# Optimization experiments

Hardware: AMD Instinct MI355X
Metric: run time of the kernel (lower is better)

Reference implementation:

```python
import jax, jax.numpy as jnp
import numpy as np

NUM_NODES = 1_000_000
H_DIM = 64
OUT_DIM = 32
NUM_RELS = 64
NUM_BASES = 4
N_SRC0 = 400_000
N_DST1 = 100_000
N_DST2 = 20_000
E1 = 600_000
E2 = 300_000


def setup_inputs() -> dict:
    key = jax.random.key(0)
    ks = jax.random.split(key, 16)
    inp = {
        "input_nodes": jax.random.randint(ks[0], (N_SRC0,), 0, NUM_NODES),
        "src1": jax.random.randint(ks[1], (E1,), 0, N_SRC0),
        "dst1": jax.random.randint(ks[2], (E1,), 0, N_DST1),
        "etype1": jax.random.randint(ks[3], (E1,), 0, NUM_RELS),
        "norm1": jax.random.uniform(ks[4], (E1, 1), dtype=jnp.float32),
        "src2": jax.random.randint(ks[5], (E2,), 0, N_DST1),
        "dst2": jax.random.randint(ks[6], (E2,), 0, N_DST2),
        "etype2": jax.random.randint(ks[7], (E2,), 0, NUM_RELS),
        "norm2": jax.random.uniform(ks[8], (E2, 1), dtype=jnp.float32),
        # learned parameters
        "emb": jax.random.normal(ks[9], (NUM_NODES, H_DIM), dtype=jnp.float32),
        "V1": jax.random.normal(ks[10], (NUM_BASES, H_DIM, H_DIM), dtype=jnp.float32) * 0.05,
        "comp1": jax.random.normal(ks[11], (NUM_RELS, NUM_BASES), dtype=jnp.float32) * 0.3,
        "b1": jnp.zeros((H_DIM,), dtype=jnp.float32),
        "V2": jax.random.normal(ks[12], (NUM_BASES, H_DIM, OUT_DIM), dtype=jnp.float32) * 0.05,
        "comp2": jax.random.normal(ks[13], (NUM_RELS, NUM_BASES), dtype=jnp.float32) * 0.3,
        "b2": jnp.zeros((OUT_DIM,), dtype=jnp.float32),
    }
    return inp


def rel_graph_conv(x, src, dst, etype, norm, V, comp, bias, n_dst):
    """Basis-decomposed RelGraphConv (no self-loop): m_e = (x[src_e] @ W_{etype_e}) * norm_e,
    with W_r = sum_b comp[r,b] V[b]; aggregate by sum into dst nodes, then add bias."""
    xe = x[src]                                 # [E, d] gather of source features
    coeff = comp[etype]                         # [E, B] relation coefficients per edge
    y = jnp.einsum('ed,bdo->ebo', xe, V)        # [E, B, o] feature x each basis
    m = jnp.einsum('ebo,eb->eo', y, coeff)      # [E, o] relation-specific message
    m = m * norm                                # per-edge normalization ([E,1] broadcast)
    h = jax.ops.segment_sum(m, dst, num_segments=n_dst)  # scatter-add to dst
    return h + bias


def reference(input_nodes, src1, dst1, etype1, norm1, src2, dst2, etype2, norm2,
              emb, V1, comp1, b1, V2, comp2, b2):
    x = emb[input_nodes]                                           # [N_src0, h]
    h = rel_graph_conv(x, src1, dst1, etype1, norm1, V1, comp1, b1, N_DST1)
    h = jax.nn.relu(h)
    out = rel_graph_conv(h, src2, dst2, etype2, norm2, V2, comp2, b2, N_DST2)
    return out
```

## Files before the change

kernel.cpp:

```cpp
#include <hip/hip_runtime.h>
#include <stdint.h>

#define NUM_NODES 1000000
#define H_DIM 64
#define OUT_DIM 32
#define NUM_RELS 64
#define NUM_BASES 4
#define N_SRC0 400000
#define N_DST1 100000
#define N_DST2 20000
#define E1 600000
#define E2 300000
#define NDST_TOT (N_DST1 + N_DST2)
#define E_TOT (E1 + E2)

typedef __attribute__((ext_vector_type(8))) short bf16x8;
typedef __attribute__((ext_vector_type(4))) float floatx4;

__device__ __forceinline__ unsigned short f2bf(float f){
  union{float f; unsigned u;} v; v.f=f;
  unsigned u=v.u;
  unsigned r=(u + 0x7FFFu + ((u>>16)&1u))>>16;
  return (unsigned short)r;
}
__device__ __forceinline__ float bf2f(unsigned short h){
  union{unsigned u; float f;} v; v.u=((unsigned)h)<<16; return v.f;
}

__global__ void k_init(const float* __restrict__ V1, const float* __restrict__ V2,
                       ushort* __restrict__ Btab1, ushort* __restrict__ Btab2,
                       int* __restrict__ deg){
  int t = blockIdx.x*blockDim.x + threadIdx.x;
  if (t < NDST_TOT) deg[t] = 0;
  if (t < 16384){
    int j = t & 7, lane = (t>>3)&63, kk = (t>>9)&7, nt = t>>12;
    int kdim = kk*32 + (lane>>4)*8 + j;
    int o = nt*16 + (lane&15);
    int k = kdim>>2, b = kdim&3;
    Btab1[t] = f2bf(V1[(b*64 + k)*64 + o]);
  } else if (t < 24576){
    int u = t - 16384;
    int j = u & 7, lane = (u>>3)&63, kk = (u>>9)&7, nt = u>>12;
    int kdim = kk*32 + (lane>>4)*8 + j;
    int o = nt*16 + (lane&15);
    int k = kdim>>2, b = kdim&3;
    Btab2[u] = f2bf(V2[(b*64 + k)*32 + o]);
  }
}

__global__ void k_hist(const int* __restrict__ dst1, const int* __restrict__ dst2,
                       int* __restrict__ deg){
  int t = blockIdx.x*blockDim.x + threadIdx.x;
  if (t < E1) atomicAdd(&deg[dst1[t]], 1);
  else if (t < E_TOT) atomicAdd(&deg[N_DST1 + dst2[t - E1]], 1);
}

__global__ void k_scan_sum(const int* __restrict__ deg, int* __restrict__ bsum, int n){
  __shared__ int lds[256];
  int tid = threadIdx.x;
  int base = blockIdx.x*1024 + tid*4;
  int s = 0;
  #pragma unroll
  for (int j=0;j<4;j++){ int i = base+j; if (i<n) s += deg[i]; }
  lds[tid] = s; __syncthreads();
  for (int off=128; off>0; off>>=1){ if (tid<off) lds[tid] += lds[tid+off]; __syncthreads(); }
  if (tid==0) bsum[blockIdx.x] = lds[0];
}

__global__ void k_scan_bsum(const int* __restrict__ bsum, int* __restrict__ boff, int nb){
  __shared__ int lds[256];
  int tid = threadIdx.x;
  int v = (tid<nb) ? bsum[tid] : 0;
  lds[tid] = v; __syncthreads();
  for (int off=1; off<256; off<<=1){
    int t = (tid>=off) ? lds[tid-off] : 0; __syncthreads();
    lds[tid] += t; __syncthreads();
  }
  if (tid<nb) boff[tid] = lds[tid] - v;
}

__global__ void k_scan_final(const int* __restrict__ deg, const int* __restrict__ boff,
                             int* __restrict__ offs, int* __restrict__ cursor, int n){
  __shared__ int lds[256];
  int tid = threadIdx.x;
  int base = blockIdx.x*1024 + tid*4;
  int a[4]; int s = 0;
  #pragma unroll
  for (int j=0;j<4;j++){ int i = base+j; a[j] = (i<n)?deg[i]:0; s += a[j]; }
  lds[tid] = s; __syncthreads();
  for (int off=1; off<256; off<<=1){
    int t = (tid>=off) ? lds[tid-off] : 0; __syncthreads();
    lds[tid] += t; __syncthreads();
  }
  int run = boff[blockIdx.x] + (lds[tid] - s);
  #pragma unroll
  for (int j=0;j<4;j++){
    int i = base+j;
    if (i<n){
      offs[i] = run; cursor[i] = run;
      run += a[j];
      if (i == n-1) offs[n] = run;
    }
  }
}

__global__ void k_scatter(const int* __restrict__ input_nodes,
                          const int* __restrict__ src1, const int* __restrict__ dst1,
                          const int* __restrict__ ety1, const float* __restrict__ nrm1,
                          const float* __restrict__ comp1,
                          const int* __restrict__ src2, const int* __restrict__ dst2,
                          const int* __restrict__ ety2, const float* __restrict__ nrm2,
                          const float* __restrict__ comp2,
                          int* __restrict__ cursor, int* __restrict__ ssrc,
                          float4* __restrict__ sc){
  int t = blockIdx.x*blockDim.x + threadIdx.x;
  int d, s, et; float nv; const float* comp;
  if (t < E1){
    d = dst1[t]; s = input_nodes[src1[t]]; et = ety1[t]; nv = nrm1[t]; comp = comp1;
  } else if (t < E_TOT){
    int e = t - E1;
    d = N_DST1 + dst2[e]; s = src2[e]; et = ety2[e]; nv = nrm2[e]; comp = comp2;
  } else return;
  int p = atomicAdd(&cursor[d], 1);
  ssrc[p] = s;
  float4 cp = ((const float4*)comp)[et];
  float4 c; c.x = cp.x*nv; c.y = cp.y*nv; c.z = cp.z*nv; c.w = cp.w*nv;
  sc[p] = c;
}


__global__ __launch_bounds__(256) void k_agg_gemm1(
    const float* __restrict__ emb, const int* __restrict__ offs,
    const int* __restrict__ ssrc, const float4* __restrict__ sc,
    const ushort* __restrict__ Btab, const float* __restrict__ bias,
    ushort* __restrict__ h_bf){
  __shared__ ushort zt[16][264];
  int lane = threadIdx.x & 63;
  int w = threadIdx.x >> 6;
  int mbase = blockIdx.x * 16;
  for (int j = 0; j < 4; j++){
    int row = w*4 + j;
    int d = mbase + row;
    int e0 = offs[d], e1 = offs[d+1];
    float a0=0.f, a1=0.f, a2=0.f, a3=0.f;
    for (int base = e0; base < e1; base += 64){
      int m = e1 - base; if (m > 64) m = 64;
      int se = 0; float4 ce = {0.f,0.f,0.f,0.f};
      if (lane < m){ se = ssrc[base + lane]; ce = sc[base + lane]; }
      int i = 0;
      for (; i + 1 < m; i += 2){
        int s0 = __shfl(se, i), s1 = __shfl(se, i+1);
        float xv0 = emb[(size_t)s0*64 + lane];
        float xv1 = emb[(size_t)s1*64 + lane];
        float c0x=__shfl(ce.x,i), c0y=__shfl(ce.y,i), c0z=__shfl(ce.z,i), c0w=__shfl(ce.w,i);
        float c1x=__shfl(ce.x,i+1), c1y=__shfl(ce.y,i+1), c1z=__shfl(ce.z,i+1), c1w=__shfl(ce.w,i+1);
        a0 = fmaf(c0x, xv0, a0); a1 = fmaf(c0y, xv0, a1);
        a2 = fmaf(c0z, xv0, a2); a3 = fmaf(c0w, xv0, a3);
        a0 = fmaf(c1x, xv1, a0); a1 = fmaf(c1y, xv1, a1);
        a2 = fmaf(c1z, xv1, a2); a3 = fmaf(c1w, xv1, a3);
      }
      if (i < m){
        int s0 = __shfl(se, i);
        float xv0 = emb[(size_t)s0*64 + lane];
        float c0x=__shfl(ce.x,i), c0y=__shfl(ce.y,i), c0z=__shfl(ce.z,i), c0w=__shfl(ce.w,i);
        a0 = fmaf(c0x, xv0, a0); a1 = fmaf(c0y, xv0, a1);
        a2 = fmaf(c0z, xv0, a2); a3 = fmaf(c0w, xv0, a3);
      }
    }
    ushort4 o; o.x=f2bf(a0); o.y=f2bf(a1); o.z=f2bf(a2); o.w=f2bf(a3);
    *(ushort4*)&zt[row][lane*4] = o;
  }
  __syncthreads();
  int quad = lane>>4, l15 = lane&15;
  bf16x8 a[8];
  #pragma unroll
  for (int kk=0; kk<8; kk++)
    a[kk] = *(const bf16x8*)&zt[l15][kk*32 + quad*8];
  floatx4 acc = {0.f,0.f,0.f,0.f};
  #pragma unroll
  for (int kk=0; kk<8; kk++){
    bf16x8 b = *((const bf16x8*)(Btab + ((w*8 + kk)*64 + lane)*8));
    acc = __builtin_amdgcn_mfma_f32_16x16x32_bf16(a[kk], b, acc, 0, 0, 0);
  }
  int col = w*16 + l15;
  float bv = bias[col];
  #pragma unroll
  for (int r=0; r<4; r++){
    int row = mbase + quad*4 + r;
    float v = fmaxf(acc[r] + bv, 0.f);
    h_bf[(size_t)row*64 + col] = f2bf(v);
  }
}

__global__ __launch_bounds__(256) void k_agg_gemm2(
    const ushort* __restrict__ hin, const int* __restrict__ offs,
    const int* __restrict__ ssrc, const float4* __restrict__ sc,
    const ushort* __restrict__ Btab, const float* __restrict__ bias,
    float* __restrict__ out){
  __shared__ ushort zt[16][264];
  int lane = threadIdx.x & 63;
  int w = threadIdx.x >> 6;
  int mbase = blockIdx.x * 16;
  for (int j = 0; j < 4; j++){
    int row = w*4 + j;
    int d = mbase + row;
    int e0 = offs[d], e1 = offs[d+1];
    float a0=0.f, a1=0.f, a2=0.f, a3=0.f;
    for (int base = e0; base < e1; base += 64){
      int m = e1 - base; if (m > 64) m = 64;
      int se = 0; float4 ce = {0.f,0.f,0.f,0.f};
      if (lane < m){ se = ssrc[base + lane]; ce = sc[base + lane]; }
      int i = 0;
      for (; i + 1 < m; i += 2){
        int s0 = __shfl(se, i), s1 = __shfl(se, i+1);
        float xv0 = bf2f(hin[(size_t)s0*64 + lane]);
        float xv1 = bf2f(hin[(size_t)s1*64 + lane]);
        float c0x=__shfl(ce.x,i), c0y=__shfl(ce.y,i), c0z=__shfl(ce.z,i), c0w=__shfl(ce.w,i);
        float c1x=__shfl(ce.x,i+1), c1y=__shfl(ce.y,i+1), c1z=__shfl(ce.z,i+1), c1w=__shfl(ce.w,i+1);
        a0 = fmaf(c0x, xv0, a0); a1 = fmaf(c0y, xv0, a1);
        a2 = fmaf(c0z, xv0, a2); a3 = fmaf(c0w, xv0, a3);
        a0 = fmaf(c1x, xv1, a0); a1 = fmaf(c1y, xv1, a1);
        a2 = fmaf(c1z, xv1, a2); a3 = fmaf(c1w, xv1, a3);
      }
      if (i < m){
        int s0 = __shfl(se, i);
        float xv0 = bf2f(hin[(size_t)s0*64 + lane]);
        float c0x=__shfl(ce.x,i), c0y=__shfl(ce.y,i), c0z=__shfl(ce.z,i), c0w=__shfl(ce.w,i);
        a0 = fmaf(c0x, xv0, a0); a1 = fmaf(c0y, xv0, a1);
        a2 = fmaf(c0z, xv0, a2); a3 = fmaf(c0w, xv0, a3);
      }
    }
    ushort4 o; o.x=f2bf(a0); o.y=f2bf(a1); o.z=f2bf(a2); o.w=f2bf(a3);
    *(ushort4*)&zt[row][lane*4] = o;
  }
  __syncthreads();
  if (w >= 2) return;
  int quad = lane>>4, l15 = lane&15;
  bf16x8 a[8];
  #pragma unroll
  for (int kk=0; kk<8; kk++)
    a[kk] = *(const bf16x8*)&zt[l15][kk*32 + quad*8];
  floatx4 acc = {0.f,0.f,0.f,0.f};
  #pragma unroll
  for (int kk=0; kk<8; kk++){
    bf16x8 b = *((const bf16x8*)(Btab + ((w*8 + kk)*64 + lane)*8));
    acc = __builtin_amdgcn_mfma_f32_16x16x32_bf16(a[kk], b, acc, 0, 0, 0);
  }
  int col = w*16 + l15;
  float bv = bias[col];
  #pragma unroll
  for (int r=0; r<4; r++){
    int row = mbase + quad*4 + r;
    out[(size_t)row*32 + col] = acc[r] + bv;
  }
}

extern "C" void kernel_launch(void* const* d_in, const int* in_sizes, int n_in,
                              void* d_out, int out_size, void* d_ws, size_t ws_size,
                              hipStream_t stream){
  const int*   input_nodes = (const int*)  d_in[0];
  const int*   src1  = (const int*)  d_in[1];
  const int*   dst1  = (const int*)  d_in[2];
  const int*   ety1  = (const int*)  d_in[3];
  const float* norm1 = (const float*)d_in[4];
  const int*   src2  = (const int*)  d_in[5];
  const int*   dst2  = (const int*)  d_in[6];
  const int*   ety2  = (const int*)  d_in[7];
  const float* norm2 = (const float*)d_in[8];
  const float* emb   = (const float*)d_in[9];
  const float* V1    = (const float*)d_in[10];
  const float* comp1 = (const float*)d_in[11];
  const float* b1    = (const float*)d_in[12];
  const float* V2    = (const float*)d_in[13];
  const float* comp2 = (const float*)d_in[14];
  const float* b2    = (const float*)d_in[15];
  float* out = (float*)d_out;

  char* p = (char*)d_ws;
  auto alloc = [&](size_t bytes)->char*{
    char* r = p; p += (bytes + 255) & ~(size_t)255; return r;
  };
  ushort* h_bf  = (ushort*)alloc((size_t)N_DST1*64*2);
  ushort* Btab1 = (ushort*)alloc(16384*2);
  ushort* Btab2 = (ushort*)alloc(8192*2);
  int* deg  = (int*)alloc((size_t)NDST_TOT*4);
  int* cur  = (int*)alloc((size_t)NDST_TOT*4);
  int* offs = (int*)alloc((size_t)(NDST_TOT+1)*4);
  int* bs   = (int*)alloc(256*4);
  int* bo   = (int*)alloc(256*4);
  int* ssrc = (int*)alloc((size_t)E_TOT*4);
  float4* sc = (float4*)alloc((size_t)E_TOT*16);

  k_init<<<(NDST_TOT + 255)/256, 256, 0, stream>>>(V1, V2, Btab1, Btab2, deg);
  k_hist<<<(E_TOT + 255)/256, 256, 0, stream>>>(dst1, dst2, deg);
  int nb = (NDST_TOT + 1023)/1024;
  k_scan_sum<<<nb, 256, 0, stream>>>(deg, bs, NDST_TOT);
  k_scan_bsum<<<1, 256, 0, stream>>>(bs, bo, nb);
  k_scan_final<<<nb, 256, 0, stream>>>(deg, bo, offs, cur, NDST_TOT);
  k_scatter<<<(E_TOT + 255)/256, 256, 0, stream>>>(input_nodes,
                                                   src1, dst1, ety1, norm1, comp1,
                                                   src2, dst2, ety2, norm2, comp2,
                                                   cur, ssrc, sc);
  k_agg_gemm1<<<N_DST1/16, 256, 0, stream>>>(emb, offs, ssrc, sc, Btab1, b1, h_bf);
  k_agg_gemm2<<<N_DST2/16, 256, 0, stream>>>(h_bf, offs + N_DST1, ssrc, sc, Btab2, b2, out);

  (void)in_sizes; (void)n_in; (void)out_size; (void)ws_size;
}
```

Measured before the change: 494.0 us.

## Assign one wave per destination row and batch eight edge gathers per iteration

The aggregation kernels now launch 1024 threads per block, so each of 16 waves handles a single destination row instead of looping over four rows. Each wave reads edge indices as wave-uniform scalar loads and issues eight independent feature-row gathers at a time, with masking for tail edges, instead of loading indices cooperatively and using shuffles. The goal is more memory-level parallelism and more waves in flight for the latency-bound gathers. In exchange, the tail masking does redundant loads, and the larger blocks leave most waves idle during the MFMA stage.

```diff
diff --git a/kernel.cpp b/kernel.cpp
--- a/kernel.cpp
+++ b/kernel.cpp
@@ -129,7 +129,7 @@
 }
 
 
-__global__ __launch_bounds__(256) void k_agg_gemm1(
+__global__ __launch_bounds__(1024) void k_agg_gemm1(
     const float* __restrict__ emb, const int* __restrict__ offs,
     const int* __restrict__ ssrc, const float4* __restrict__ sc,
     const ushort* __restrict__ Btab, const float* __restrict__ bias,
@@ -138,61 +138,63 @@
   int lane = threadIdx.x & 63;
   int w = threadIdx.x >> 6;
   int mbase = blockIdx.x * 16;
-  for (int j = 0; j < 4; j++){
-    int row = w*4 + j;
-    int d = mbase + row;
-    int e0 = offs[d], e1 = offs[d+1];
-    float a0=0.f, a1=0.f, a2=0.f, a3=0.f;
-    for (int base = e0; base < e1; base += 64){
-      int m = e1 - base; if (m > 64) m = 64;
-      int se = 0; float4 ce = {0.f,0.f,0.f,0.f};
-      if (lane < m){ se = ssrc[base + lane]; ce = sc[base + lane]; }
-      int i = 0;
-      for (; i + 1 < m; i += 2){
-        int s0 = __shfl(se, i), s1 = __shfl(se, i+1);
-        float xv0 = emb[(size_t)s0*64 + lane];
-        float xv1 = emb[(size_t)s1*64 + lane];
-        float c0x=__shfl(ce.x,i), c0y=__shfl(ce.y,i), c0z=__shfl(ce.z,i), c0w=__shfl(ce.w,i);
-        float c1x=__shfl(ce.x,i+1), c1y=__shfl(ce.y,i+1), c1z=__shfl(ce.z,i+1), c1w=__shfl(ce.w,i+1);
-        a0 = fmaf(c0x, xv0, a0); a1 = fmaf(c0y, xv0, a1);
-        a2 = fmaf(c0z, xv0, a2); a3 = fmaf(c0w, xv0, a3);
-        a0 = fmaf(c1x, xv1, a0); a1 = fmaf(c1y, xv1, a1);
-        a2 = fmaf(c1z, xv1, a2); a3 = fmaf(c1w, xv1, a3);
-      }
-      if (i < m){
-        int s0 = __shfl(se, i);
-        float xv0 = emb[(size_t)s0*64 + lane];
-        float c0x=__shfl(ce.x,i), c0y=__shfl(ce.y,i), c0z=__shfl(ce.z,i), c0w=__shfl(ce.w,i);
-        a0 = fmaf(c0x, xv0, a0); a1 = fmaf(c0y, xv0, a1);
-        a2 = fmaf(c0z, xv0, a2); a3 = fmaf(c0w, xv0, a3);
-      }
-    }
-    ushort4 o; o.x=f2bf(a0); o.y=f2bf(a1); o.z=f2bf(a2); o.w=f2bf(a3);
-    *(ushort4*)&zt[row][lane*4] = o;
-  }
+  int d = mbase + w;
+  int e0 = __builtin_amdgcn_readfirstlane(offs[d]);
+  int e1 = __builtin_amdgcn_readfirstlane(offs[d+1]);
+  float a0=0.f, a1=0.f, a2=0.f, a3=0.f;
+  for (int e = e0; e < e1; e += 8){
+    int idx[8]; float msk[8];
+    #pragma unroll
+    for (int k=0;k<8;k++){
+      int t = e + k;
+      idx[k] = (t < e1) ? t : e0;
+      msk[k] = (t < e1) ? 1.f : 0.f;
+    }
+    int s[8]; float4 c[8];
+    #pragma unroll
+    for (int k=0;k<8;k++){
+      s[k] = __builtin_amdgcn_readfirstlane(ssrc[idx[k]]);
+      c[k] = sc[idx[k]];
+    }
+    float x[8];
+    #pragma unroll
+    for (int k=0;k<8;k++)
+      x[k] = emb[(size_t)s[k]*64 + lane] * msk[k];
+    #pragma unroll
+    for (int k=0;k<8;k++){
+      a0 = fmaf(c[k].x, x[k], a0);
+      a1 = fmaf(c[k].y, x[k], a1);
+      a2 = fmaf(c[k].z, x[k], a2);
+      a3 = fmaf(c[k].w, x[k], a3);
+    }
+  }
+  ushort4 o; o.x=f2bf(a0); o.y=f2bf(a1); o.z=f2bf(a2); o.w=f2bf(a3);
+  *(ushort4*)&zt[w][lane*4] = o;
   __syncthreads();
-  int quad = lane>>4, l15 = lane&15;
-  bf16x8 a[8];
-  #pragma unroll
-  for (int kk=0; kk<8; kk++)
-    a[kk] = *(const bf16x8*)&zt[l15][kk*32 + quad*8];
-  floatx4 acc = {0.f,0.f,0.f,0.f};
-  #pragma unroll
-  for (int kk=0; kk<8; kk++){
-    bf16x8 b = *((const bf16x8*)(Btab + ((w*8 + kk)*64 + lane)*8));
-    acc = __builtin_amdgcn_mfma_f32_16x16x32_bf16(a[kk], b, acc, 0, 0, 0);
-  }
-  int col = w*16 + l15;
-  float bv = bias[col];
-  #pragma unroll
-  for (int r=0; r<4; r++){
-    int row = mbase + quad*4 + r;
-    float v = fmaxf(acc[r] + bv, 0.f);
-    h_bf[(size_t)row*64 + col] = f2bf(v);
-  }
-}
-
-__global__ __launch_bounds__(256) void k_agg_gemm2(
+  if (w < 4){
+    int quad = lane>>4, l15 = lane&15;
+    bf16x8 a[8];
+    #pragma unroll
+    for (int kk=0; kk<8; kk++)
+      a[kk] = *(const bf16x8*)&zt[l15][kk*32 + quad*8];
+    floatx4 acc = {0.f,0.f,0.f,0.f};
+    #pragma unroll
+    for (int kk=0; kk<8; kk++){
+      bf16x8 b = *((const bf16x8*)(Btab + ((w*8 + kk)*64 + lane)*8));
+      acc = __builtin_amdgcn_mfma_f32_16x16x32_bf16(a[kk], b, acc, 0, 0, 0);
+    }
+    int col = w*16 + l15;
+    float bv = bias[col];
+    #pragma unroll
+    for (int r=0; r<4; r++){
+      int row = mbase + quad*4 + r;
+      float v = fmaxf(acc[r] + bv, 0.f);
+      h_bf[(size_t)row*64 + col] = f2bf(v);
+    }
+  }
+}
+
+__global__ __launch_bounds__(1024) void k_agg_gemm2(
     const ushort* __restrict__ hin, const int* __restrict__ offs,
     const int* __restrict__ ssrc, const float4* __restrict__ sc,
     const ushort* __restrict__ Btab, const float* __restrict__ bias,
@@ -201,57 +203,58 @@
   int lane = threadIdx.x & 63;
   int w = threadIdx.x >> 6;
   int mbase = blockIdx.x * 16;
-  for (int j = 0; j < 4; j++){
-    int row = w*4 + j;
-    int d = mbase + row;
-    int e0 = offs[d], e1 = offs[d+1];
-    float a0=0.f, a1=0.f, a2=0.f, a3=0.f;
-    for (int base = e0; base < e1; base += 64){
-      int m = e1 - base; if (m > 64) m = 64;
-      int se = 0; float4 ce = {0.f,0.f,0.f,0.f};
-      if (lane < m){ se = ssrc[base + lane]; ce = sc[base + lane]; }
-      int i = 0;
-      for (; i + 1 < m; i += 2){
-        int s0 = __shfl(se, i), s1 = __shfl(se, i+1);
-        float xv0 = bf2f(hin[(size_t)s0*64 + lane]);
-        float xv1 = bf2f(hin[(size_t)s1*64 + lane]);
-        float c0x=__shfl(ce.x,i), c0y=__shfl(ce.y,i), c0z=__shfl(ce.z,i), c0w=__shfl(ce.w,i);
-        float c1x=__shfl(ce.x,i+1), c1y=__shfl(ce.y,i+1), c1z=__shfl(ce.z,i+1), c1w=__shfl(ce.w,i+1);
-        a0 = fmaf(c0x, xv0, a0); a1 = fmaf(c0y, xv0, a1);
-        a2 = fmaf(c0z, xv0, a2); a3 = fmaf(c0w, xv0, a3);
-        a0 = fmaf(c1x, xv1, a0); a1 = fmaf(c1y, xv1, a1);
-        a2 = fmaf(c1z, xv1, a2); a3 = fmaf(c1w, xv1, a3);
-      }
-      if (i < m){
-        int s0 = __shfl(se, i);
-        float xv0 = bf2f(hin[(size_t)s0*64 + lane]);
-        float c0x=__shfl(ce.x,i), c0y=__shfl(ce.y,i), c0z=__shfl(ce.z,i), c0w=__shfl(ce.w,i);
-        a0 = fmaf(c0x, xv0, a0); a1 = fmaf(c0y, xv0, a1);
-        a2 = fmaf(c0z, xv0, a2); a3 = fmaf(c0w, xv0, a3);
-      }
-    }
-    ushort4 o; o.x=f2bf(a0); o.y=f2bf(a1); o.z=f2bf(a2); o.w=f2bf(a3);
-    *(ushort4*)&zt[row][lane*4] = o;
-  }
+  int d = mbase + w;
+  int e0 = __builtin_amdgcn_readfirstlane(offs[d]);
+  int e1 = __builtin_amdgcn_readfirstlane(offs[d+1]);
+  float a0=0.f, a1=0.f, a2=0.f, a3=0.f;
+  for (int e = e0; e < e1; e += 8){
+    int idx[8]; float msk[8];
+    #pragma unroll
+    for (int k=0;k<8;k++){
+      int t = e + k;
+      idx[k] = (t < e1) ? t : e0;
+      msk[k] = (t < e1) ? 1.f : 0.f;
+    }
+    int s[8]; float4 c[8];
+    #pragma unroll
+    for (int k=0;k<8;k++){
+      s[k] = __builtin_amdgcn_readfirstlane(ssrc[idx[k]]);
+      c[k] = sc[idx[k]];
+    }
+    float x[8];
+    #pragma unroll
+    for (int k=0;k<8;k++)
+      x[k] = bf2f(hin[(size_t)s[k]*64 + lane]) * msk[k];
+    #pragma unroll
+    for (int k=0;k<8;k++){
+      a0 = fmaf(c[k].x, x[k], a0);
+      a1 = fmaf(c[k].y, x[k], a1);
+      a2 = fmaf(c[k].z, x[k], a2);
+      a3 = fmaf(c[k].w, x[k], a3);
+    }
+  }
+  ushort4 o; o.x=f2bf(a0); o.y=f2bf(a1); o.z=f2bf(a2); o.w=f2bf(a3);
+  *(ushort4*)&zt[w][lane*4] = o;
   __syncthreads();
-  if (w >= 2) return;
-  int quad = lane>>4, l15 = lane&15;
-  bf16x8 a[8];
-  #pragma unroll
-  for (int kk=0; kk<8; kk++)
-    a[kk] = *(const bf16x8*)&zt[l15][kk*32 + quad*8];
-  floatx4 acc = {0.f,0.f,0.f,0.f};
-  #pragma unroll
-  for (int kk=0; kk<8; kk++){
-    bf16x8 b = *((const bf16x8*)(Btab + ((w*8 + kk)*64 + lane)*8));
-    acc = __builtin_amdgcn_mfma_f32_16x16x32_bf16(a[kk], b, acc, 0, 0, 0);
-  }
-  int col = w*16 + l15;
-  float bv = bias[col];
-  #pragma unroll
-  for (int r=0; r<4; r++){
-    int row = mbase + quad*4 + r;
-    out[(size_t)row*32 + col] = acc[r] + bv;
+  if (w < 2){
+    int quad = lane>>4, l15 = lane&15;
+    bf16x8 a[8];
+    #pragma unroll
+    for (int kk=0; kk<8; kk++)
+      a[kk] = *(const bf16x8*)&zt[l15][kk*32 + quad*8];
+    floatx4 acc = {0.f,0.f,0.f,0.f};
+    #pragma unroll
+    for (int kk=0; kk<8; kk++){
+      bf16x8 b = *((const bf16x8*)(Btab + ((w*8 + kk)*64 + lane)*8));
+      acc = __builtin_amdgcn_mfma_f32_16x16x32_bf16(a[kk], b, acc, 0, 0, 0);
+    }
+    int col = w*16 + l15;
+    float bv = bias[col];
+    #pragma unroll
+    for (int r=0; r<4; r++){
+      int row = mbase + quad*4 + r;
+      out[(size_t)row*32 + col] = acc[r] + bv;
+    }
   }
 }
 
@@ -301,8 +304,8 @@
                                                    src1, dst1, ety1, norm1, comp1,
                                                    src2, dst2, ety2, norm2, comp2,
                                                    cur, ssrc, sc);
-  k_agg_gemm1<<<N_DST1/16, 256, 0, stream>>>(emb, offs, ssrc, sc, Btab1, b1, h_bf);
-  k_agg_gemm2<<<N_DST2/16, 256, 0, stream>>>(h_bf, offs + N_DST1, ssrc, sc, Btab2, b2, out);
+  k_agg_gemm1<<<N_DST1/16, 1024, 0, stream>>>(emb, offs, ssrc, sc, Btab1, b1, h_bf);
+  k_agg_gemm2<<<N_DST2/16, 1024, 0, stream>>>(h_bf, offs + N_DST1, ssrc, sc, Btab2, b2, out);
 
   (void)in_sizes; (void)n_in; (void)out_size; (void)ws_size;
 }
```

Measured after the change: 481.1 us. 1.03x faster.
